# Performance work log

Measured on AMD Instinct MI355X. Metric: run time of the kernel, lower is better.

## Reference

```python
import jax, jax.numpy as jnp
import numpy as np

KSIZE = 3
KN = (KSIZE - 1) // 2  # 1
TEMP = 50.0


def _extract_patches(x, same_pad):
    """TF tf.image.extract_patches ordering: per location, (dy, dx, channel).
    x: [b,H,W,d] -> [b,h,w,9*d] (h=H,w=W if same_pad else H-2,W-2)."""
    if same_pad:
        x = jnp.pad(x, ((0, 0), (KN, KN), (KN, KN), (0, 0)))
    b, Hp, Wp, d = x.shape
    h, w = Hp - 2 * KN, Wp - 2 * KN
    slices = [x[:, dy:dy + h, dx:dx + w, :]
              for dy in range(KSIZE) for dx in range(KSIZE)]
    return jnp.concatenate(slices, axis=-1)


def setup_inputs() -> dict:
    key = jax.random.key(0)
    k1, k2, k3 = jax.random.split(key, 3)
    b, h, w, dims = 4, 48, 48, 64
    g_in = jax.random.normal(k1, (b, h, w, dims), dtype=jnp.float32)
    # binary inpainting mask (1 = known background, 0 = hole)
    mask = (jax.random.uniform(k2, (b, h, w, 1)) > 0.5).astype(jnp.float32)
    W2 = jax.random.normal(k3, (2 * dims, dims), dtype=jnp.float32) / np.sqrt(2.0 * dims)
    b2 = jnp.zeros((dims,), dtype=jnp.float32)
    return {"g_in": g_in, "mask": mask, "W2": W2, "b2": b2}


def reference(g_in, mask, W2, b2):
    b, h, w, dims = g_in.shape
    c = (h - 2 * KN) * (w - 2 * KN)

    mask_r = mask  # already (h,w,1); broadcasts over dims (== tile)
    bg = g_in * mask_r

    # p1: VALID 3x3 patches of bg -> dynamic kernels, [b, c, 9*dims]
    p1 = _extract_patches(bg, same_pad=False).reshape(b, c, KSIZE * KSIZE * dims)
    # p2: SAME 3x3 patches of g_in, [b, h, w, 9*dims]
    p2 = _extract_patches(g_in, same_pad=True)

    # cross-correlation: conv2d(ft, k1) == per-location dot with each bg patch
    CS = jnp.einsum('byxk,bjk->byxj', p2, p1)              # [b,h,w,c]
    k1d = jnp.sum(p1 * p1, axis=2)                          # [b,c]
    wwd = jnp.sum(p2 * p2, axis=3, keepdims=True)           # [b,h,w,1]
    DS1 = k1d[:, None, None, :] + wwd - 2.0 * CS            # squared distances
    mu = jnp.mean(DS1, axis=3, keepdims=True)
    sd = jnp.std(DS1, axis=3, keepdims=True)                # population std (tf.math.reduce_std)
    DS2 = -jnp.tanh((DS1 - mu) / sd)
    CA = jax.nn.softmax(TEMP * DS2, axis=-1)                # [b,h,w,c]

    # transposed conv aggregation with per-sample kernels k2[b,j,dy,dx,ch]
    k2 = p1.reshape(b, c, KSIZE, KSIZE, dims)
    CA_pad = jnp.pad(CA, ((0, 0), (KN, KN), (KN, KN), (0, 0)))
    acl = jnp.zeros((b, h, w, dims), dtype=g_in.dtype)
    for dy in range(KSIZE):
        for dx in range(KSIZE):
            win = CA_pad[:, 2 * KN - dy:2 * KN - dy + h, 2 * KN - dx:2 * KN - dx + w, :]
            acl = acl + jnp.einsum('byxj,bjd->byxd', win, k2[:, :, dy, dx, :])
    acl = acl / 9.0

    ACL = bg + acl * (1.0 - mask_r)
    con1 = jnp.concatenate([g_in, ACL], axis=3)             # [b,h,w,2*dims]
    return jax.nn.elu(jnp.einsum('byxk,kd->byxd', con1, W2) + b2)
```

## Files before the change

kernel.cpp:

```cpp
#include <hip/hip_runtime.h>
#include <hip/hip_fp16.h>
#include <math.h>

#define BB 4
#define HH 48
#define WW 48
#define DD 64
#define CH 46
#define CWp 46
#define CC (CH*CWp)
#define KK 576
#define HWp (HH*WW)
#define KPAD 2176
#define KSPLIT0 1088

typedef __attribute__((ext_vector_type(8))) short short8;
typedef __attribute__((ext_vector_type(4))) float float4v;

#define OFFB_P1H  ((size_t)0)
#define OFFB_P2H  ((size_t)9750528)
#define OFFB_P1T  ((size_t)20367360)
#define OFFB_K1D  ((size_t)30394368)
#define OFFB_S    ((size_t)30428224)
#define OFFB_AGG0 ((size_t)70536256)
#define OFFB_AGG1 ((size_t)81153088)

__device__ __forceinline__ ushort f2bf(float x) {
    unsigned u = __float_as_uint(x);
    return (ushort)((u + 0x7FFFu + ((u >> 16) & 1u)) >> 16);
}

__device__ __forceinline__ float waveReduceSum(float x) {
#pragma unroll
    for (int o = 32; o > 0; o >>= 1) x += __shfl_down(x, o, 64);
    return x;
}

__device__ __forceinline__ float blockReduceSum(float x, float* sm) {
#pragma unroll
    for (int o = 32; o > 0; o >>= 1) x += __shfl_down(x, o, 64);
    int lane = threadIdx.x & 63, w = threadIdx.x >> 6;
    __syncthreads();
    if (lane == 0) sm[w] = x;
    __syncthreads();
    return sm[0] + sm[1] + sm[2] + sm[3];
}

__device__ __forceinline__ float fast_tanh(float z) {
    float e = __expf(2.f * z);
    return 1.f - 2.f / (e + 1.f);
}

typedef __attribute__((address_space(3))) void lds_void_t;
typedef __attribute__((address_space(1))) void gmem_void_t;
__device__ __forceinline__ void gld16(const ushort* g, ushort* lds) {
    __builtin_amdgcn_global_load_lds((gmem_void_t*)g, (lds_void_t*)lds, 16, 0, 0);
}

__global__ __launch_bounds__(256) void build_p2(const float* __restrict__ g,
                                                ushort* __restrict__ p2h) {
    int pix = blockIdx.x * 4 + (threadIdx.x >> 6);
    int b = pix / HWp, yx = pix % HWp;
    int y = yx / WW, x = yx % WW;
    int c = threadIdx.x & 63;
    const float* gb = g + (size_t)b * HWp * DD;
    ushort* dst = p2h + (size_t)pix * KK;
#pragma unroll
    for (int dy = 0; dy < 3; dy++) {
#pragma unroll
        for (int dx = 0; dx < 3; dx++) {
            int yy = y + dy - 1, xx = x + dx - 1;
            float v = (yy >= 0 && yy < HH && xx >= 0 && xx < WW)
                          ? gb[((size_t)yy * WW + xx) * DD + c] : 0.f;
            dst[(dy * 3 + dx) * DD + c] = f2bf(v);
        }
    }
}

__global__ __launch_bounds__(256) void build_p1(const float* __restrict__ g,
                                                const float* __restrict__ mask,
                                                ushort* __restrict__ p1h,
                                                float* __restrict__ k1d) {
    int j = blockIdx.x * 4 + (threadIdx.x >> 6);
    int b = j / CC, jj = j % CC;
    int jy = jj / CWp, jx = jj % CWp;
    int c = threadIdx.x & 63;
    const float* gb = g + (size_t)b * HWp * DD;
    const float* mb = mask + (size_t)b * HWp;
    ushort* dst = p1h + (size_t)j * KK;
    float ss = 0.f;
#pragma unroll
    for (int dy = 0; dy < 3; dy++) {
#pragma unroll
        for (int dx = 0; dx < 3; dx++) {
            int p = (jy + dy) * WW + (jx + dx);
            float v = gb[(size_t)p * DD + c] * mb[p];
            dst[(dy * 3 + dx) * DD + c] = f2bf(v);
            ss += v * v;
        }
    }
    ss = waveReduceSum(ss);
    if (c == 0) k1d[j] = ss;
}

__global__ __launch_bounds__(256) void transpose_p1(const ushort* __restrict__ p1h,
                                                    ushort* __restrict__ p1t) {
    __shared__ ushort T[64 * 65];
    int b = blockIdx.z;
    int j0 = blockIdx.x * 64;
    int c0 = blockIdx.y * 64;
    const ushort* src = p1h + (size_t)b * CC * KK;
    ushort* dst = p1t + (size_t)b * KK * KPAD;
    int t = threadIdx.x;
#pragma unroll
    for (int pass = 0; pass < 2; pass++) {
        int v = t + pass * 256;
        int r = v >> 3, c8 = (v & 7) * 8;
        int j = j0 + r;
        uint4 d = make_uint4(0, 0, 0, 0);
        if (j < CC) d = *(const uint4*)(src + (size_t)j * KK + c0 + c8);
        ushort tmp[8];
        *(uint4*)tmp = d;
#pragma unroll
        for (int u = 0; u < 8; u++) T[r * 65 + c8 + u] = tmp[u];
    }
    __syncthreads();
#pragma unroll
    for (int pass = 0; pass < 2; pass++) {
        int v = t + pass * 256;
        int cr = v >> 3, j8 = (v & 7) * 8;
        ushort tmp[8];
#pragma unroll
        for (int u = 0; u < 8; u++) tmp[u] = T[(j8 + u) * 65 + cr];
        *(uint4*)(dst + (size_t)(c0 + cr) * KPAD + j0 + j8) = *(uint4*)tmp;
    }
}

template <int NBI, bool NMASK>
__device__ __forceinline__ void gemm_tile64(const ushort* __restrict__ Ab,
                                            const ushort* __restrict__ Bb,
                                            int lda, int ldb, int kb, int ke,
                                            int Nrem,
                                            ushort* As, ushort* Bs,
                                            float4v (&acc)[4][NBI]) {
    int tid = threadIdx.x;
    int l = tid & 63, w = tid >> 6;
    int quad = l >> 4, l15 = l & 15;
    int sw = l15 & 7;
    int wm = (w >> 1) * 64, wn = (w & 1) * (NBI * 16);
    int sr = l >> 3;
    int gch = (l & 7) ^ (sr & 7);

    for (int k0 = kb; k0 < ke; k0 += 64) {
#pragma unroll
        for (int i = 0; i < 4; i++) {
            int rg = 4 * w + i;
            int r = rg * 8 + sr;
            gld16(Ab + (size_t)r * lda + k0 + gch * 8, As + rg * 512);
        }
#pragma unroll
        for (int i = 0; i < NBI; i++) {
            int rg = NBI * w + i;
            int r = rg * 8 + sr;
            if (!NMASK || r < Nrem)
                gld16(Bb + (size_t)r * ldb + k0 + gch * 8, Bs + rg * 512);
        }
        __syncthreads();

#pragma unroll
        for (int h = 0; h < 2; h++) {
            short8 af[4], bf[NBI];
#pragma unroll
            for (int i = 0; i < 4; i++)
                af[i] = *(const short8*)&As[(wm + i * 16 + l15) * 64 + ((h * 4 + quad) ^ sw) * 8];
#pragma unroll
            for (int j = 0; j < NBI; j++)
                bf[j] = *(const short8*)&Bs[(wn + j * 16 + l15) * 64 + ((h * 4 + quad) ^ sw) * 8];
#pragma unroll
            for (int i = 0; i < 4; i++)
#pragma unroll
                for (int j = 0; j < NBI; j++)
                    acc[i][j] = __builtin_amdgcn_mfma_f32_16x16x32_bf16(af[i], bf[j], acc[i][j], 0, 0, 0);
        }
        __syncthreads();
    }
}

__global__ __launch_bounds__(256) void gemm1_nt(const ushort* __restrict__ A,
                                                const ushort* __restrict__ Bt,
                                                __half* __restrict__ Cout) {
    __shared__ ushort As[128 * 64];
    __shared__ ushort Bs[128 * 64];
    int i0 = blockIdx.x;
    int b = (i0 & 7) >> 1;
    int tile = ((i0 >> 3) << 1) | (i0 & 1);
    int ty = tile / 17, tx = tile - ty * 17;
    int m0 = ty * 128, n0 = tx * 128;
    const ushort* Ab = A + (size_t)b * HWp * KK + (size_t)m0 * KK;
    const ushort* Bb = Bt + (size_t)b * CC * KK + (size_t)n0 * KK;
    float4v acc[4][4];
#pragma unroll
    for (int i = 0; i < 4; i++)
#pragma unroll
        for (int j = 0; j < 4; j++) acc[i][j] = (float4v){0.f, 0.f, 0.f, 0.f};

    gemm_tile64<4, true>(Ab, Bb, KK, KK, 0, KK, CC - n0, As, Bs, acc);

    int tid = threadIdx.x;
    int lane = tid & 63, wid = tid >> 6;
    int quad = lane >> 4, l15 = lane & 15;
    int wm = (wid >> 1) * 64, wn = (wid & 1) * 64;
    __half* C = Cout + (size_t)b * HWp * KPAD;
#pragma unroll
    for (int i = 0; i < 4; i++) {
#pragma unroll
        for (int j = 0; j < 4; j++) {
            int n = n0 + wn + j * 16 + l15;
            if (n < CC) {
#pragma unroll
                for (int r = 0; r < 4; r++) {
                    int m = m0 + wm + i * 16 + quad * 4 + r;
                    C[(size_t)m * KPAD + n] = __float2half(acc[i][j][r]);
                }
            }
        }
    }
}

__global__ __launch_bounds__(256) void gemm2_split(const ushort* __restrict__ A,
                                                   const ushort* __restrict__ Bt,
                                                   __half* __restrict__ agg0,
                                                   __half* __restrict__ agg1) {
    __shared__ ushort As[128 * 64];
    __shared__ ushort Bs[192 * 64];
    int i0 = blockIdx.x;
    int z = i0 & 7;
    int b = z >> 1, split = z & 1;
    int tile = i0 >> 3;
    int ty = tile / 3, tx = tile - ty * 3;
    int m0 = ty * 128, n0 = tx * 192;
    const ushort* Ab = A + (size_t)b * HWp * KPAD + (size_t)m0 * KPAD;
    const ushort* Bb = Bt + (size_t)b * KK * KPAD + (size_t)n0 * KPAD;
    float4v acc[4][6];
#pragma unroll
    for (int i = 0; i < 4; i++)
#pragma unroll
        for (int j = 0; j < 6; j++) acc[i][j] = (float4v){0.f, 0.f, 0.f, 0.f};

    gemm_tile64<6, false>(Ab, Bb, KPAD, KPAD, split ? KSPLIT0 : 0,
                          split ? KPAD : KSPLIT0, 192, As, Bs, acc);

    int tid = threadIdx.x;
    int lane = tid & 63, wid = tid >> 6;
    int quad = lane >> 4, l15 = lane & 15;
    int wm = (wid >> 1) * 64, wn = (wid & 1) * 96;
    __half* C = (split ? agg1 : agg0) + (size_t)b * HWp * KK;
#pragma unroll
    for (int i = 0; i < 4; i++) {
#pragma unroll
        for (int j = 0; j < 6; j++) {
            int n = n0 + wn + j * 16 + l15;
#pragma unroll
            for (int r = 0; r < 4; r++) {
                int m = m0 + wm + i * 16 + quad * 4 + r;
                C[(size_t)m * KK + n] = __float2half(acc[i][j][r]);
            }
        }
    }
}

__global__ __launch_bounds__(256) void rowsoft(void* __restrict__ Sbase,
                                               const float* __restrict__ k1d) {
    __shared__ float sm[4];
    size_t row = blockIdx.x;
    int b = (int)(row / HWp);
    const __half* p = (const __half*)Sbase + row * KPAD;
    ushort* wout = (ushort*)Sbase + row * KPAD;
    const float* k1 = k1d + (size_t)b * CC;
    int tid = threadIdx.x;
    float v[9];
#pragma unroll
    for (int i = 0; i < 9; i++) {
        int idx = tid + i * 256;
        v[i] = (idx < CC) ? (k1[idx] - 2.f * __half2float(p[idx])) : 0.f;
    }
    float s = 0.f;
#pragma unroll
    for (int i = 0; i < 9; i++) { int idx = tid + i * 256; if (idx < CC) s += v[i]; }
    s = blockReduceSum(s, sm);
    float mu = s / (float)CC;
    float vs = 0.f;
#pragma unroll
    for (int i = 0; i < 9; i++) {
        int idx = tid + i * 256;
        if (idx < CC) { float d = v[i] - mu; vs += d * d; }
    }
    vs = blockReduceSum(vs, sm);
    float inv_sd = 1.f / sqrtf(vs / (float)CC);
    float es = 0.f;
#pragma unroll
    for (int i = 0; i < 9; i++) {
        int idx = tid + i * 256;
        if (idx < CC) {
            v[i] = __expf(-50.f * fast_tanh((v[i] - mu) * inv_sd));
            es += v[i];
        }
    }
    es = blockReduceSum(es, sm);
    float invz = 1.f / es;
#pragma unroll
    for (int i = 0; i < 9; i++) {
        int idx = tid + i * 256;
        if (idx < KPAD) wout[idx] = (idx < CC) ? f2bf(v[i] * invz) : (ushort)0;
    }
}

__global__ __launch_bounds__(256) void final_k(const float* __restrict__ g,
                                               const float* __restrict__ mask,
                                               const __half* __restrict__ agg0,
                                               const __half* __restrict__ agg1,
                                               const float* __restrict__ W2,
                                               const float* __restrict__ b2,
                                               float* __restrict__ out) {
    int w = threadIdx.x >> 6, d = threadIdx.x & 63;
    int pix = blockIdx.x * 4 + w;
    int b = pix / HWp, yx = pix % HWp;
    int y = yx / WW, x = yx % WW;

    __shared__ float con1[4][128];
    float acl = 0.f;
#pragma unroll
    for (int dy = 0; dy < 3; dy++) {
#pragma unroll
        for (int dx = 0; dx < 3; dx++) {
            int yy = y + 1 - dy, xx = x + 1 - dx;
            if (yy >= 0 && yy < HH && xx >= 0 && xx < WW) {
                size_t off = ((size_t)(b * HWp + yy * WW + xx)) * KK + (dy * 3 + dx) * DD + d;
                acl += __half2float(agg0[off]) + __half2float(agg1[off]);
            }
        }
    }
    float m = mask[pix];
    float gv = g[(size_t)pix * DD + d];
    float bgv = gv * m;
    float ACL = bgv + (acl / 9.f) * (1.f - m);
    con1[w][d] = gv;
    con1[w][64 + d] = ACL;
    __syncthreads();
    float accv = b2[d];
#pragma unroll 8
    for (int k = 0; k < 128; k++) accv = fmaf(con1[w][k], W2[k * 64 + d], accv);
    out[(size_t)pix * DD + d] = accv > 0.f ? accv : expm1f(accv);
}

extern "C" void kernel_launch(void* const* d_in, const int* in_sizes, int n_in,
                              void* d_out, int out_size, void* d_ws, size_t ws_size,
                              hipStream_t stream) {
    const float* g    = (const float*)d_in[0];
    const float* mask = (const float*)d_in[1];
    const float* W2   = (const float*)d_in[2];
    const float* b2   = (const float*)d_in[3];
    float* out = (float*)d_out;
    char* ws = (char*)d_ws;

    ushort* p1h  = (ushort*)(ws + OFFB_P1H);
    ushort* p2h  = (ushort*)(ws + OFFB_P2H);
    ushort* p1t  = (ushort*)(ws + OFFB_P1T);
    float*  k1d  = (float*) (ws + OFFB_K1D);
    void*   S    = (void*)  (ws + OFFB_S);
    __half* agg0 = (__half*)(ws + OFFB_AGG0);
    __half* agg1 = (__half*)(ws + OFFB_AGG1);

    build_p2<<<BB * HWp / 4, 256, 0, stream>>>(g, p2h);
    build_p1<<<BB * CC / 4, 256, 0, stream>>>(g, mask, p1h, k1d);
    transpose_p1<<<dim3(34, 9, BB), 256, 0, stream>>>(p1h, p1t);

    gemm1_nt<<<dim3(1224), 256, 0, stream>>>(p2h, p1h, (__half*)S);

    rowsoft<<<BB * HWp, 256, 0, stream>>>(S, k1d);

    gemm2_split<<<dim3(432), 256, 0, stream>>>((const ushort*)S, p1t, agg0, agg1);

    final_k<<<BB * HWp / 4, 256, 0, stream>>>(g, mask, agg0, agg1, W2, b2, out);
}
```

Measured before the change: 194.5 us.

## Double-buffer GEMM K-loop, merge patch builders, vectorize row softmax

The shared GEMM tile routine becomes a double-buffered loop with a K-step of 32: the next slice is fetched into LDS via global_load_lds while MFMAs run on the current one, and there is one barrier per step instead of two. The two patch-building kernels are merged into a single launch, saving one launch. The row-softmax kernel now reads and writes 8 contiguous elements per thread with vector loads instead of strided scalar access. The smaller K step means more loop iterations and barriers, and the added buffers increase LDS use, which may lower occupancy.

```diff
diff --git a/kernel.cpp b/kernel.cpp
--- a/kernel.cpp
+++ b/kernel.cpp
@@ -57,50 +57,49 @@
     __builtin_amdgcn_global_load_lds((gmem_void_t*)g, (lds_void_t*)lds, 16, 0, 0);
 }
 
-__global__ __launch_bounds__(256) void build_p2(const float* __restrict__ g,
-                                                ushort* __restrict__ p2h) {
-    int pix = blockIdx.x * 4 + (threadIdx.x >> 6);
-    int b = pix / HWp, yx = pix % HWp;
-    int y = yx / WW, x = yx % WW;
-    int c = threadIdx.x & 63;
-    const float* gb = g + (size_t)b * HWp * DD;
-    ushort* dst = p2h + (size_t)pix * KK;
-#pragma unroll
-    for (int dy = 0; dy < 3; dy++) {
-#pragma unroll
-        for (int dx = 0; dx < 3; dx++) {
-            int yy = y + dy - 1, xx = x + dx - 1;
-            float v = (yy >= 0 && yy < HH && xx >= 0 && xx < WW)
-                          ? gb[((size_t)yy * WW + xx) * DD + c] : 0.f;
-            dst[(dy * 3 + dx) * DD + c] = f2bf(v);
-        }
-    }
-}
-
-__global__ __launch_bounds__(256) void build_p1(const float* __restrict__ g,
-                                                const float* __restrict__ mask,
-                                                ushort* __restrict__ p1h,
-                                                float* __restrict__ k1d) {
-    int j = blockIdx.x * 4 + (threadIdx.x >> 6);
-    int b = j / CC, jj = j % CC;
-    int jy = jj / CWp, jx = jj % CWp;
-    int c = threadIdx.x & 63;
-    const float* gb = g + (size_t)b * HWp * DD;
-    const float* mb = mask + (size_t)b * HWp;
-    ushort* dst = p1h + (size_t)j * KK;
-    float ss = 0.f;
-#pragma unroll
-    for (int dy = 0; dy < 3; dy++) {
-#pragma unroll
-        for (int dx = 0; dx < 3; dx++) {
-            int p = (jy + dy) * WW + (jx + dx);
-            float v = gb[(size_t)p * DD + c] * mb[p];
-            dst[(dy * 3 + dx) * DD + c] = f2bf(v);
-            ss += v * v;
-        }
-    }
-    ss = waveReduceSum(ss);
-    if (c == 0) k1d[j] = ss;
+__global__ __launch_bounds__(256) void build_patches(const float* __restrict__ g,
+                                                     const float* __restrict__ mask,
+                                                     ushort* __restrict__ p2h,
+                                                     ushort* __restrict__ p1h,
+                                                     float* __restrict__ k1d) {
+    int w = threadIdx.x >> 6, c = threadIdx.x & 63;
+    if (blockIdx.x < (BB * HWp / 4)) {
+        int pix = blockIdx.x * 4 + w;
+        int b = pix / HWp, yx = pix % HWp;
+        int y = yx / WW, x = yx % WW;
+        const float* gb = g + (size_t)b * HWp * DD;
+        ushort* dst = p2h + (size_t)pix * KK;
+#pragma unroll
+        for (int dy = 0; dy < 3; dy++) {
+#pragma unroll
+            for (int dx = 0; dx < 3; dx++) {
+                int yy = y + dy - 1, xx = x + dx - 1;
+                float v = (yy >= 0 && yy < HH && xx >= 0 && xx < WW)
+                              ? gb[((size_t)yy * WW + xx) * DD + c] : 0.f;
+                dst[(dy * 3 + dx) * DD + c] = f2bf(v);
+            }
+        }
+    } else {
+        int j = (blockIdx.x - BB * HWp / 4) * 4 + w;
+        int b = j / CC, jj = j % CC;
+        int jy = jj / CWp, jx = jj % CWp;
+        const float* gb = g + (size_t)b * HWp * DD;
+        const float* mb = mask + (size_t)b * HWp;
+        ushort* dst = p1h + (size_t)j * KK;
+        float ss = 0.f;
+#pragma unroll
+        for (int dy = 0; dy < 3; dy++) {
+#pragma unroll
+            for (int dx = 0; dx < 3; dx++) {
+                int p = (jy + dy) * WW + (jx + dx);
+                float v = gb[(size_t)p * DD + c] * mb[p];
+                dst[(dy * 3 + dx) * DD + c] = f2bf(v);
+                ss += v * v;
+            }
+        }
+        ss = waveReduceSum(ss);
+        if (c == 0) k1d[j] = ss;
+    }
 }
 
 __global__ __launch_bounds__(256) void transpose_p1(const ushort* __restrict__ p1h,
@@ -136,61 +135,79 @@
     }
 }
 
-template <int NBI, bool NMASK>
-__device__ __forceinline__ void gemm_tile64(const ushort* __restrict__ Ab,
-                                            const ushort* __restrict__ Bb,
-                                            int lda, int ldb, int kb, int ke,
-                                            int Nrem,
-                                            ushort* As, ushort* Bs,
-                                            float4v (&acc)[4][NBI]) {
+template <int NF, bool NMASK>
+__device__ __forceinline__ void gemm_tile_db(const ushort* __restrict__ Ab,
+                                             const ushort* __restrict__ Bb,
+                                             int lda, int ldb, int kb, int ke,
+                                             int Nrem,
+                                             ushort* As, ushort* Bs,
+                                             float4v (&acc)[4][NF]) {
+    constexpr int NBI = NF / 2;
+    constexpr int BBUF = 2048 * NBI;
     int tid = threadIdx.x;
     int l = tid & 63, w = tid >> 6;
     int quad = l >> 4, l15 = l & 15;
-    int sw = l15 & 7;
-    int wm = (w >> 1) * 64, wn = (w & 1) * (NBI * 16);
-    int sr = l >> 3;
-    int gch = (l & 7) ^ (sr & 7);
-
-    for (int k0 = kb; k0 < ke; k0 += 64) {
-#pragma unroll
-        for (int i = 0; i < 4; i++) {
-            int rg = 4 * w + i;
-            int r = rg * 8 + sr;
-            gld16(Ab + (size_t)r * lda + k0 + gch * 8, As + rg * 512);
-        }
-#pragma unroll
-        for (int i = 0; i < NBI; i++) {
-            int rg = NBI * w + i;
-            int r = rg * 8 + sr;
-            if (!NMASK || r < Nrem)
-                gld16(Bb + (size_t)r * ldb + k0 + gch * 8, Bs + rg * 512);
-        }
+    int sw8 = (l15 >> 1) & 3;
+    int wm = (w >> 1) * 64, wn = (w & 1) * (NF * 16);
+    int rowInC = l >> 2;
+    int cSw = (l & 3) ^ ((l >> 3) & 3);
+
+#pragma unroll
+    for (int i = 0; i < 2; i++) {
+        int rg = w * 2 + i;
+        gld16(Ab + (size_t)(rg * 16 + rowInC) * lda + kb + cSw * 8, As + rg * 512);
+    }
+#pragma unroll
+    for (int i = 0; i < NBI; i++) {
+        int rg = w * NBI + i;
+        int r = rg * 16 + rowInC;
+        if (!NMASK || r < Nrem)
+            gld16(Bb + (size_t)r * ldb + kb + cSw * 8, Bs + rg * 512);
+    }
+
+    int buf = 0;
+    for (int k0 = kb; k0 < ke; k0 += 32) {
         __syncthreads();
-
-#pragma unroll
-        for (int h = 0; h < 2; h++) {
-            short8 af[4], bf[NBI];
-#pragma unroll
-            for (int i = 0; i < 4; i++)
-                af[i] = *(const short8*)&As[(wm + i * 16 + l15) * 64 + ((h * 4 + quad) ^ sw) * 8];
-#pragma unroll
-            for (int j = 0; j < NBI; j++)
-                bf[j] = *(const short8*)&Bs[(wn + j * 16 + l15) * 64 + ((h * 4 + quad) ^ sw) * 8];
-#pragma unroll
-            for (int i = 0; i < 4; i++)
-#pragma unroll
-                for (int j = 0; j < NBI; j++)
-                    acc[i][j] = __builtin_amdgcn_mfma_f32_16x16x32_bf16(af[i], bf[j], acc[i][j], 0, 0, 0);
-        }
-        __syncthreads();
+        int nb = buf ^ 1;
+        if (k0 + 32 < ke) {
+#pragma unroll
+            for (int i = 0; i < 2; i++) {
+                int rg = w * 2 + i;
+                gld16(Ab + (size_t)(rg * 16 + rowInC) * lda + (k0 + 32) + cSw * 8,
+                      As + nb * 4096 + rg * 512);
+            }
+#pragma unroll
+            for (int i = 0; i < NBI; i++) {
+                int rg = w * NBI + i;
+                int r = rg * 16 + rowInC;
+                if (!NMASK || r < Nrem)
+                    gld16(Bb + (size_t)r * ldb + (k0 + 32) + cSw * 8,
+                          Bs + nb * BBUF + rg * 512);
+            }
+        }
+        const ushort* Ax = As + buf * 4096;
+        const ushort* Bx = Bs + buf * BBUF;
+        short8 af[4], bf[NF];
+#pragma unroll
+        for (int i = 0; i < 4; i++)
+            af[i] = *(const short8*)&Ax[(wm + i * 16 + l15) * 32 + ((quad ^ sw8)) * 8];
+#pragma unroll
+        for (int j = 0; j < NF; j++)
+            bf[j] = *(const short8*)&Bx[(wn + j * 16 + l15) * 32 + ((quad ^ sw8)) * 8];
+#pragma unroll
+        for (int i = 0; i < 4; i++)
+#pragma unroll
+            for (int j = 0; j < NF; j++)
+                acc[i][j] = __builtin_amdgcn_mfma_f32_16x16x32_bf16(af[i], bf[j], acc[i][j], 0, 0, 0);
+        buf = nb;
     }
 }
 
 __global__ __launch_bounds__(256) void gemm1_nt(const ushort* __restrict__ A,
                                                 const ushort* __restrict__ Bt,
                                                 __half* __restrict__ Cout) {
-    __shared__ ushort As[128 * 64];
-    __shared__ ushort Bs[128 * 64];
+    __shared__ ushort As[2 * 4096];
+    __shared__ ushort Bs[2 * 4096];
     int i0 = blockIdx.x;
     int b = (i0 & 7) >> 1;
     int tile = ((i0 >> 3) << 1) | (i0 & 1);
@@ -204,7 +221,7 @@
 #pragma unroll
         for (int j = 0; j < 4; j++) acc[i][j] = (float4v){0.f, 0.f, 0.f, 0.f};
 
-    gemm_tile64<4, true>(Ab, Bb, KK, KK, 0, KK, CC - n0, As, Bs, acc);
+    gemm_tile_db<4, true>(Ab, Bb, KK, KK, 0, KK, CC - n0, As, Bs, acc);
 
     int tid = threadIdx.x;
     int lane = tid & 63, wid = tid >> 6;
@@ -231,8 +248,8 @@
                                                    const ushort* __restrict__ Bt,
                                                    __half* __restrict__ agg0,
                                                    __half* __restrict__ agg1) {
-    __shared__ ushort As[128 * 64];
-    __shared__ ushort Bs[192 * 64];
+    __shared__ ushort As[2 * 4096];
+    __shared__ ushort Bs[2 * 6144];
     int i0 = blockIdx.x;
     int z = i0 & 7;
     int b = z >> 1, split = z & 1;
@@ -247,8 +264,8 @@
 #pragma unroll
         for (int j = 0; j < 6; j++) acc[i][j] = (float4v){0.f, 0.f, 0.f, 0.f};
 
-    gemm_tile64<6, false>(Ab, Bb, KPAD, KPAD, split ? KSPLIT0 : 0,
-                          split ? KPAD : KSPLIT0, 192, As, Bs, acc);
+    gemm_tile_db<6, false>(Ab, Bb, KPAD, KPAD, split ? KSPLIT0 : 0,
+                           split ? KPAD : KSPLIT0, 192, As, Bs, acc);
 
     int tid = threadIdx.x;
     int lane = tid & 63, wid = tid >> 6;
@@ -277,41 +294,67 @@
     const __half* p = (const __half*)Sbase + row * KPAD;
     ushort* wout = (ushort*)Sbase + row * KPAD;
     const float* k1 = k1d + (size_t)b * CC;
-    int tid = threadIdx.x;
-    float v[9];
-#pragma unroll
-    for (int i = 0; i < 9; i++) {
-        int idx = tid + i * 256;
-        v[i] = (idx < CC) ? (k1[idx] - 2.f * __half2float(p[idx])) : 0.f;
+    int t = threadIdx.x;
+    bool hasx = t < 34;
+
+    uint4 raw = *(const uint4*)(p + t * 8);
+    uint rx = hasx ? *(const uint*)(p + 2048 + t * 2) : 0u;
+    float v[8], vx[2];
+    {
+        const __half2* h2 = (const __half2*)&raw;
+#pragma unroll
+        for (int i = 0; i < 4; i++) {
+            float2 f = __half22float2(h2[i]);
+            v[2 * i] = f.x; v[2 * i + 1] = f.y;
+        }
+        __half2 hx = *(__half2*)&rx;
+        float2 fx = __half22float2(hx);
+        vx[0] = fx.x; vx[1] = fx.y;
+    }
+    {
+        const float* kp = k1 + t * 8;
+#pragma unroll
+        for (int i = 0; i < 8; i++) v[i] = kp[i] - 2.f * v[i];
+        if (hasx) {
+            vx[0] = k1[2048 + t * 2] - 2.f * vx[0];
+            vx[1] = k1[2048 + t * 2 + 1] - 2.f * vx[1];
+        }
     }
     float s = 0.f;
 #pragma unroll
-    for (int i = 0; i < 9; i++) { int idx = tid + i * 256; if (idx < CC) s += v[i]; }
+    for (int i = 0; i < 8; i++) s += v[i];
+    if (hasx) s += vx[0] + vx[1];
     s = blockReduceSum(s, sm);
     float mu = s / (float)CC;
     float vs = 0.f;
 #pragma unroll
-    for (int i = 0; i < 9; i++) {
-        int idx = tid + i * 256;
-        if (idx < CC) { float d = v[i] - mu; vs += d * d; }
-    }
+    for (int i = 0; i < 8; i++) { float d = v[i] - mu; vs += d * d; }
+    if (hasx) { float d0 = vx[0] - mu, d1 = vx[1] - mu; vs += d0 * d0 + d1 * d1; }
     vs = blockReduceSum(vs, sm);
     float inv_sd = 1.f / sqrtf(vs / (float)CC);
     float es = 0.f;
 #pragma unroll
-    for (int i = 0; i < 9; i++) {
-        int idx = tid + i * 256;
-        if (idx < CC) {
-            v[i] = __expf(-50.f * fast_tanh((v[i] - mu) * inv_sd));
-            es += v[i];
-        }
+    for (int i = 0; i < 8; i++) {
+        v[i] = __expf(-50.f * fast_tanh((v[i] - mu) * inv_sd));
+        es += v[i];
+    }
+    if (hasx) {
+        vx[0] = __expf(-50.f * fast_tanh((vx[0] - mu) * inv_sd));
+        vx[1] = __expf(-50.f * fast_tanh((vx[1] - mu) * inv_sd));
+        es += vx[0] + vx[1];
     }
     es = blockReduceSum(es, sm);
     float invz = 1.f / es;
-#pragma unroll
-    for (int i = 0; i < 9; i++) {
-        int idx = tid + i * 256;
-        if (idx < KPAD) wout[idx] = (idx < CC) ? f2bf(v[i] * invz) : (ushort)0;
+
+    ushort o[8];
+#pragma unroll
+    for (int i = 0; i < 8; i++) o[i] = f2bf(v[i] * invz);
+    *(uint4*)(wout + t * 8) = *(const uint4*)o;
+    if (hasx) {
+        ushort ox[2] = { f2bf(vx[0] * invz), f2bf(vx[1] * invz) };
+        *(uint*)(wout + 2048 + t * 2) = *(const uint*)ox;
+    } else {
+        *(uint*)(wout + CC + 2 * (t - 34)) = 0u;
     }
 }
 
@@ -371,8 +414,7 @@
     __half* agg0 = (__half*)(ws + OFFB_AGG0);
     __half* agg1 = (__half*)(ws + OFFB_AGG1);
 
-    build_p2<<<BB * HWp / 4, 256, 0, stream>>>(g, p2h);
-    build_p1<<<BB * CC / 4, 256, 0, stream>>>(g, mask, p1h, k1d);
+    build_patches<<<BB * HWp / 4 + BB * CC / 4, 256, 0, stream>>>(g, mask, p2h, p1h, k1d);
     transpose_p1<<<dim3(34, 9, BB), 256, 0, stream>>>(p1h, p1t);
 
     gemm1_nt<<<dim3(1224), 256, 0, stream>>>(p2h, p1h, (__half*)S);
```

New measurement: 192.8 us. Within noise of the previous version (-0.9%).
